# Kernel tuning notes

Measured on AMD Instinct MI355X. Metric: run time of the kernel, lower is better.

## Reference

```python
import jax, jax.numpy as jnp
import numpy as np


def setup_inputs() -> dict:
    key = jax.random.key(0)
    k1, k2, k3 = jax.random.split(key, 3)
    B, S, Q, K, D = 64, 512, 800, 4, 64
    q_data = jax.random.normal(k1, (B, S, Q), dtype=jnp.float32)
    r_data = jax.random.randint(k2, (B, S), 0, K)
    # learned params (xavier-ish scale)
    Wq = jax.random.normal(k3, (D, Q), dtype=jnp.float32) * (0.5 * (2.0 / (Q + D)) ** 0.5)
    bq = jnp.zeros((D,), dtype=jnp.float32)
    Wr = jax.random.normal(jax.random.fold_in(key, 7), (1, K), dtype=jnp.float32) * (0.5 * (2.0 / (K + 1)) ** 0.5)
    br = jnp.zeros((1,), dtype=jnp.float32)
    return {"q_data": q_data, "r_data": r_data, "Wq": Wq, "bq": bq,
            "Wr": Wr, "br": br, "n_questions": Q, "n_cats": K}


def reference(q_data, r_data, Wq, bq, Wr, br, n_questions, n_cats):
    # Vectorized over (batch, seq): original looped over t in python.
    K = n_cats
    k_idx = jnp.arange(K, dtype=q_data.dtype)                      # [K]
    dist = jnp.abs(k_idx[None, None, :] - r_data[..., None].astype(q_data.dtype)) / (K - 1)  # [B,S,K]
    weights = jnp.maximum(1.0 - dist, 0.0)                        # [B,S,K]
    # response_weights: Linear(K -> 1) then sigmoid -> scalar gate per (b,s)
    gate = jax.nn.sigmoid(jnp.einsum('bsk,ok->bso', weights, Wr) + br)  # [B,S,1]
    weighted_q = q_data * gate                                    # [B,S,Q]
    # question_embed: Linear(Q -> D)
    out = jnp.einsum('bsq,dq->bsd', weighted_q, Wq) + bq          # [B,S,D]
    return out
```

## Files before the change

### kernel.cpp

```cpp
#include <hip/hip_runtime.h>
#include <hip/hip_bf16.h>


#define QD 800
#define DD 64
#define M_TOTAL 32768
#define KT 25
#define DEPTH 5

typedef __attribute__((ext_vector_type(8))) short bf16x8;
typedef __attribute__((ext_vector_type(4))) float f32x4;

static __device__ __forceinline__ short f2bf(float f) {
  union { __hip_bfloat16 h; short s; } u;
  u.h = __float2bfloat16(f);
  return u.s;
}

static __device__ __forceinline__ bf16x8 pack8(f32x4 lo, f32x4 hi) {
  bf16x8 r;
  r[0] = f2bf(lo.x); r[1] = f2bf(lo.y); r[2] = f2bf(lo.z); r[3] = f2bf(lo.w);
  r[4] = f2bf(hi.x); r[5] = f2bf(hi.y); r[6] = f2bf(hi.z); r[7] = f2bf(hi.w);
  return r;
}

static __device__ __forceinline__ bf16x8 load_split8(const float* __restrict__ p) {
  return pack8(*reinterpret_cast<const f32x4*>(p),
               *reinterpret_cast<const f32x4*>(p + 16));
}

static __device__ __forceinline__ f32x4 ntload4(const float* __restrict__ p) {
  return __builtin_nontemporal_load(reinterpret_cast<const f32x4*>(p));
}

__global__ void convert_wq_kernel(const float* __restrict__ Wq, short* __restrict__ Bb) {
  int idx = blockIdx.x * 256 + threadIdx.x;
  int kt = idx >> 8;
  int acc = (idx >> 6) & 3;
  int lane = idx & 63;
  int l15 = lane & 15, lhi = lane >> 4;
  const float* p = Wq + (acc * 16 + l15) * QD + kt * 32 + lhi * 4;
  *reinterpret_cast<bf16x8*>(Bb + (size_t)idx * 8) = load_split8(p);
}

__global__ __launch_bounds__(256, 2) void sold_kernel(
    const float* __restrict__ q, const int* __restrict__ rdat,
    const short* __restrict__ Bb, const float* __restrict__ bq,
    const float* __restrict__ Wr, const float* __restrict__ br,
    float* __restrict__ out) {
  const int lane = threadIdx.x & 63;
  const int wave = threadIdx.x >> 6;
  const int l15 = lane & 15;
  const int lhi = lane >> 4;
  const int m0 = blockIdx.x * 64 + wave * 16;

  const float* ap = q + (size_t)(m0 + l15) * QD + lhi * 4;
  const short* bp = Bb + (size_t)lane * 8;

  f32x4 aLo[DEPTH], aHi[DEPTH];
  bf16x8 bfr[DEPTH][4];

#pragma unroll
  for (int s = 0; s < DEPTH; ++s) {
    const float* a = ap + s * 32;
    aLo[s] = ntload4(a);
    aHi[s] = ntload4(a + 16);
    const short* p = bp + s * 2048;
    bfr[s][0] = *reinterpret_cast<const bf16x8*>(p + 0 * 512);
    bfr[s][1] = *reinterpret_cast<const bf16x8*>(p + 1 * 512);
    bfr[s][2] = *reinterpret_cast<const bf16x8*>(p + 2 * 512);
    bfr[s][3] = *reinterpret_cast<const bf16x8*>(p + 3 * 512);
  }

  f32x4 acc0 = {0.f, 0.f, 0.f, 0.f};
  f32x4 acc1 = {0.f, 0.f, 0.f, 0.f};
  f32x4 acc2 = {0.f, 0.f, 0.f, 0.f};
  f32x4 acc3 = {0.f, 0.f, 0.f, 0.f};

#pragma unroll
  for (int kt = 0; kt < KT; ++kt) {
    const int s = kt % DEPTH;
    bf16x8 a = pack8(aLo[s], aHi[s]);
    acc0 = __builtin_amdgcn_mfma_f32_16x16x32_bf16(a, bfr[s][0], acc0, 0, 0, 0);
    acc1 = __builtin_amdgcn_mfma_f32_16x16x32_bf16(a, bfr[s][1], acc1, 0, 0, 0);
    acc2 = __builtin_amdgcn_mfma_f32_16x16x32_bf16(a, bfr[s][2], acc2, 0, 0, 0);
    acc3 = __builtin_amdgcn_mfma_f32_16x16x32_bf16(a, bfr[s][3], acc3, 0, 0, 0);
    const int nx = kt + DEPTH;
    if (nx < KT) {
      const float* a2 = ap + nx * 32;
      aLo[s] = ntload4(a2);
      aHi[s] = ntload4(a2 + 16);
      const short* p = bp + nx * 2048;
      bfr[s][0] = *reinterpret_cast<const bf16x8*>(p + 0 * 512);
      bfr[s][1] = *reinterpret_cast<const bf16x8*>(p + 1 * 512);
      bfr[s][2] = *reinterpret_cast<const bf16x8*>(p + 2 * 512);
      bfr[s][3] = *reinterpret_cast<const bf16x8*>(p + 3 * 512);
    }
    __builtin_amdgcn_sched_barrier(0);
  }

  float wr[4] = {Wr[0], Wr[1], Wr[2], Wr[3]};
  float brv = br[0];
  float lut[4];
  const float inv3 = 1.0f / 3.0f;
#pragma unroll
  for (int r = 0; r < 4; ++r) {
    float s = brv;
#pragma unroll
    for (int k = 0; k < 4; ++k) {
      float w = fmaxf(1.0f - fabsf((float)(k - r)) * inv3, 0.0f);
      s += w * wr[k];
    }
    lut[r] = 1.0f / (1.0f + __expf(-s));
  }

  float bqv0 = bq[0 * 16 + l15];
  float bqv1 = bq[1 * 16 + l15];
  float bqv2 = bq[2 * 16 + l15];
  float bqv3 = bq[3 * 16 + l15];

#pragma unroll
  for (int r = 0; r < 4; ++r) {
    int row = m0 + lhi * 4 + r;
    float g = lut[rdat[row]];
    float* orow = out + (size_t)row * DD + l15;
    __builtin_nontemporal_store(acc0[r] * g + bqv0, orow + 0);
    __builtin_nontemporal_store(acc1[r] * g + bqv1, orow + 16);
    __builtin_nontemporal_store(acc2[r] * g + bqv2, orow + 32);
    __builtin_nontemporal_store(acc3[r] * g + bqv3, orow + 48);
  }
}

__global__ __launch_bounds__(256, 2) void sold_direct(
    const float* __restrict__ q, const int* __restrict__ rdat,
    const float* __restrict__ Wq, const float* __restrict__ bq,
    const float* __restrict__ Wr, const float* __restrict__ br,
    float* __restrict__ out) {
  const int lane = threadIdx.x & 63;
  const int wave = threadIdx.x >> 6;
  const int l15 = lane & 15;
  const int lhi = lane >> 4;
  const int m0 = blockIdx.x * 64 + wave * 16;
  const float* aptr = q + (size_t)(m0 + l15) * QD + lhi * 4;
  const float* w0 = Wq + (0 * 16 + l15) * QD + lhi * 4;
  const float* w1 = Wq + (1 * 16 + l15) * QD + lhi * 4;
  const float* w2 = Wq + (2 * 16 + l15) * QD + lhi * 4;
  const float* w3 = Wq + (3 * 16 + l15) * QD + lhi * 4;
  f32x4 acc0 = {0.f,0.f,0.f,0.f}, acc1 = {0.f,0.f,0.f,0.f};
  f32x4 acc2 = {0.f,0.f,0.f,0.f}, acc3 = {0.f,0.f,0.f,0.f};
#pragma unroll 5
  for (int kt = 0; kt < KT; ++kt) {
    bf16x8 a  = load_split8(aptr + kt * 32);
    bf16x8 b0 = load_split8(w0 + kt * 32);
    bf16x8 b1 = load_split8(w1 + kt * 32);
    bf16x8 b2 = load_split8(w2 + kt * 32);
    bf16x8 b3 = load_split8(w3 + kt * 32);
    acc0 = __builtin_amdgcn_mfma_f32_16x16x32_bf16(a, b0, acc0, 0, 0, 0);
    acc1 = __builtin_amdgcn_mfma_f32_16x16x32_bf16(a, b1, acc1, 0, 0, 0);
    acc2 = __builtin_amdgcn_mfma_f32_16x16x32_bf16(a, b2, acc2, 0, 0, 0);
    acc3 = __builtin_amdgcn_mfma_f32_16x16x32_bf16(a, b3, acc3, 0, 0, 0);
  }
  float wr[4] = {Wr[0], Wr[1], Wr[2], Wr[3]};
  float brv = br[0], lut[4];
  const float inv3 = 1.0f / 3.0f;
#pragma unroll
  for (int r = 0; r < 4; ++r) {
    float s = brv;
#pragma unroll
    for (int k = 0; k < 4; ++k)
      s += fmaxf(1.0f - fabsf((float)(k - r)) * inv3, 0.0f) * wr[k];
    lut[r] = 1.0f / (1.0f + __expf(-s));
  }
  float bqv0 = bq[l15], bqv1 = bq[16 + l15], bqv2 = bq[32 + l15], bqv3 = bq[48 + l15];
#pragma unroll
  for (int r = 0; r < 4; ++r) {
    int row = m0 + lhi * 4 + r;
    float g = lut[rdat[row]];
    float* orow = out + (size_t)row * DD + l15;
    orow[0]  = acc0[r] * g + bqv0;
    orow[16] = acc1[r] * g + bqv1;
    orow[32] = acc2[r] * g + bqv2;
    orow[48] = acc3[r] * g + bqv3;
  }
}

extern "C" void kernel_launch(void* const* d_in, const int* in_sizes, int n_in,
                              void* d_out, int out_size, void* d_ws, size_t ws_size,
                              hipStream_t stream) {
  const float* q    = (const float*)d_in[0];
  const int*   rdat = (const int*)d_in[1];
  const float* Wq   = (const float*)d_in[2];
  const float* bq   = (const float*)d_in[3];
  const float* Wr   = (const float*)d_in[4];
  const float* br   = (const float*)d_in[5];
  float* out = (float*)d_out;

  const size_t need_ws = (size_t)KT * 2048 * sizeof(short);
  if (ws_size >= need_ws) {
    short* Bb = (short*)d_ws;
    convert_wq_kernel<<<KT, 256, 0, stream>>>(Wq, Bb);
    sold_kernel<<<M_TOTAL / 64, 256, 0, stream>>>(q, rdat, Bb, bq, Wr, br, out);
  } else {
    sold_direct<<<M_TOTAL / 64, 256, 0, stream>>>(q, rdat, Wq, bq, Wr, br, out);
  }
}
```

Measured before the change: 168.1 us.

## Stage bf16 Wq in LDS per block and drop the separate convert kernel

Removes the separate Wq-to-bf16 conversion kernel and its workspace buffer. Each 512-thread block now converts the whole Wq into LDS (100KB) itself, then streams B fragments from LDS with a 3-deep register prefetch while A keeps its 5-deep global prefetch. Block size and rows per block double to 128, which removes one launch and the global B reloads. The cost is that every block repeats the Wq conversion plus a sync before compute, and the large LDS footprint limits blocks per CU.

```diff
diff --git a/kernel.cpp b/kernel.cpp
--- a/kernel.cpp
+++ b/kernel.cpp
@@ -7,6 +7,7 @@
 #define M_TOTAL 32768
 #define KT 25
 #define DEPTH 5
+#define NCHUNK (KT * 4 * 64)
 
 typedef __attribute__((ext_vector_type(8))) short bf16x8;
 typedef __attribute__((ext_vector_type(4))) float f32x4;
@@ -33,44 +34,52 @@
   return __builtin_nontemporal_load(reinterpret_cast<const f32x4*>(p));
 }
 
-__global__ void convert_wq_kernel(const float* __restrict__ Wq, short* __restrict__ Bb) {
-  int idx = blockIdx.x * 256 + threadIdx.x;
-  int kt = idx >> 8;
-  int acc = (idx >> 6) & 3;
-  int lane = idx & 63;
-  int l15 = lane & 15, lhi = lane >> 4;
-  const float* p = Wq + (acc * 16 + l15) * QD + kt * 32 + lhi * 4;
-  *reinterpret_cast<bf16x8*>(Bb + (size_t)idx * 8) = load_split8(p);
-}
-
-__global__ __launch_bounds__(256, 2) void sold_kernel(
+__global__ __launch_bounds__(512, 2) void sold_lds(
     const float* __restrict__ q, const int* __restrict__ rdat,
-    const short* __restrict__ Bb, const float* __restrict__ bq,
+    const float* __restrict__ Wq, const float* __restrict__ bq,
     const float* __restrict__ Wr, const float* __restrict__ br,
     float* __restrict__ out) {
-  const int lane = threadIdx.x & 63;
-  const int wave = threadIdx.x >> 6;
+  __shared__ short Bs[NCHUNK * 8];
+
+  const int tid = threadIdx.x;
+
+#pragma unroll
+  for (int it = 0; it < 13; ++it) {
+    int idx = tid + it * 512;
+    if (idx < NCHUNK) {
+      int kt = idx >> 8;
+      int acc = (idx >> 6) & 3;
+      int cl = idx & 63;
+      int l15 = cl & 15, lhi = cl >> 4;
+      const float* p = Wq + (acc * 16 + l15) * QD + kt * 32 + lhi * 4;
+      *reinterpret_cast<bf16x8*>(&Bs[(size_t)idx * 8]) = load_split8(p);
+    }
+  }
+  __syncthreads();
+
+  const int lane = tid & 63;
+  const int wave = tid >> 6;
   const int l15 = lane & 15;
   const int lhi = lane >> 4;
-  const int m0 = blockIdx.x * 64 + wave * 16;
+  const int m0 = blockIdx.x * 128 + wave * 16;
 
   const float* ap = q + (size_t)(m0 + l15) * QD + lhi * 4;
-  const short* bp = Bb + (size_t)lane * 8;
+  const short* bp = Bs + lane * 8;
 
   f32x4 aLo[DEPTH], aHi[DEPTH];
-  bf16x8 bfr[DEPTH][4];
-
 #pragma unroll
   for (int s = 0; s < DEPTH; ++s) {
     const float* a = ap + s * 32;
     aLo[s] = ntload4(a);
     aHi[s] = ntload4(a + 16);
-    const short* p = bp + s * 2048;
-    bfr[s][0] = *reinterpret_cast<const bf16x8*>(p + 0 * 512);
-    bfr[s][1] = *reinterpret_cast<const bf16x8*>(p + 1 * 512);
-    bfr[s][2] = *reinterpret_cast<const bf16x8*>(p + 2 * 512);
-    bfr[s][3] = *reinterpret_cast<const bf16x8*>(p + 3 * 512);
   }
+
+  bf16x8 bb[3][4];
+#pragma unroll
+  for (int t = 0; t < 2; ++t)
+#pragma unroll
+    for (int j = 0; j < 4; ++j)
+      bb[t][j] = *reinterpret_cast<const bf16x8*>(bp + t * 2048 + j * 512);
 
   f32x4 acc0 = {0.f, 0.f, 0.f, 0.f};
   f32x4 acc1 = {0.f, 0.f, 0.f, 0.f};
@@ -79,22 +88,24 @@
 
 #pragma unroll
   for (int kt = 0; kt < KT; ++kt) {
-    const int s = kt % DEPTH;
-    bf16x8 a = pack8(aLo[s], aHi[s]);
-    acc0 = __builtin_amdgcn_mfma_f32_16x16x32_bf16(a, bfr[s][0], acc0, 0, 0, 0);
-    acc1 = __builtin_amdgcn_mfma_f32_16x16x32_bf16(a, bfr[s][1], acc1, 0, 0, 0);
-    acc2 = __builtin_amdgcn_mfma_f32_16x16x32_bf16(a, bfr[s][2], acc2, 0, 0, 0);
-    acc3 = __builtin_amdgcn_mfma_f32_16x16x32_bf16(a, bfr[s][3], acc3, 0, 0, 0);
+    const int cur = kt % 3;
+    const int pf = kt + 2;
+    if (pf < KT) {
+      const int dst = pf % 3;
+#pragma unroll
+      for (int j = 0; j < 4; ++j)
+        bb[dst][j] = *reinterpret_cast<const bf16x8*>(bp + pf * 2048 + j * 512);
+    }
+    bf16x8 a = pack8(aLo[kt % DEPTH], aHi[kt % DEPTH]);
+    acc0 = __builtin_amdgcn_mfma_f32_16x16x32_bf16(a, bb[cur][0], acc0, 0, 0, 0);
+    acc1 = __builtin_amdgcn_mfma_f32_16x16x32_bf16(a, bb[cur][1], acc1, 0, 0, 0);
+    acc2 = __builtin_amdgcn_mfma_f32_16x16x32_bf16(a, bb[cur][2], acc2, 0, 0, 0);
+    acc3 = __builtin_amdgcn_mfma_f32_16x16x32_bf16(a, bb[cur][3], acc3, 0, 0, 0);
     const int nx = kt + DEPTH;
     if (nx < KT) {
       const float* a2 = ap + nx * 32;
-      aLo[s] = ntload4(a2);
-      aHi[s] = ntload4(a2 + 16);
-      const short* p = bp + nx * 2048;
-      bfr[s][0] = *reinterpret_cast<const bf16x8*>(p + 0 * 512);
-      bfr[s][1] = *reinterpret_cast<const bf16x8*>(p + 1 * 512);
-      bfr[s][2] = *reinterpret_cast<const bf16x8*>(p + 2 * 512);
-      bfr[s][3] = *reinterpret_cast<const bf16x8*>(p + 3 * 512);
+      aLo[kt % DEPTH] = ntload4(a2);
+      aHi[kt % DEPTH] = ntload4(a2 + 16);
     }
     __builtin_amdgcn_sched_barrier(0);
   }
@@ -131,59 +142,6 @@
   }
 }
 
-__global__ __launch_bounds__(256, 2) void sold_direct(
-    const float* __restrict__ q, const int* __restrict__ rdat,
-    const float* __restrict__ Wq, const float* __restrict__ bq,
-    const float* __restrict__ Wr, const float* __restrict__ br,
-    float* __restrict__ out) {
-  const int lane = threadIdx.x & 63;
-  const int wave = threadIdx.x >> 6;
-  const int l15 = lane & 15;
-  const int lhi = lane >> 4;
-  const int m0 = blockIdx.x * 64 + wave * 16;
-  const float* aptr = q + (size_t)(m0 + l15) * QD + lhi * 4;
-  const float* w0 = Wq + (0 * 16 + l15) * QD + lhi * 4;
-  const float* w1 = Wq + (1 * 16 + l15) * QD + lhi * 4;
-  const float* w2 = Wq + (2 * 16 + l15) * QD + lhi * 4;
-  const float* w3 = Wq + (3 * 16 + l15) * QD + lhi * 4;
-  f32x4 acc0 = {0.f,0.f,0.f,0.f}, acc1 = {0.f,0.f,0.f,0.f};
-  f32x4 acc2 = {0.f,0.f,0.f,0.f}, acc3 = {0.f,0.f,0.f,0.f};
-#pragma unroll 5
-  for (int kt = 0; kt < KT; ++kt) {
-    bf16x8 a  = load_split8(aptr + kt * 32);
-    bf16x8 b0 = load_split8(w0 + kt * 32);
-    bf16x8 b1 = load_split8(w1 + kt * 32);
-    bf16x8 b2 = load_split8(w2 + kt * 32);
-    bf16x8 b3 = load_split8(w3 + kt * 32);
-    acc0 = __builtin_amdgcn_mfma_f32_16x16x32_bf16(a, b0, acc0, 0, 0, 0);
-    acc1 = __builtin_amdgcn_mfma_f32_16x16x32_bf16(a, b1, acc1, 0, 0, 0);
-    acc2 = __builtin_amdgcn_mfma_f32_16x16x32_bf16(a, b2, acc2, 0, 0, 0);
-    acc3 = __builtin_amdgcn_mfma_f32_16x16x32_bf16(a, b3, acc3, 0, 0, 0);
-  }
-  float wr[4] = {Wr[0], Wr[1], Wr[2], Wr[3]};
-  float brv = br[0], lut[4];
-  const float inv3 = 1.0f / 3.0f;
-#pragma unroll
-  for (int r = 0; r < 4; ++r) {
-    float s = brv;
-#pragma unroll
-    for (int k = 0; k < 4; ++k)
-      s += fmaxf(1.0f - fabsf((float)(k - r)) * inv3, 0.0f) * wr[k];
-    lut[r] = 1.0f / (1.0f + __expf(-s));
-  }
-  float bqv0 = bq[l15], bqv1 = bq[16 + l15], bqv2 = bq[32 + l15], bqv3 = bq[48 + l15];
-#pragma unroll
-  for (int r = 0; r < 4; ++r) {
-    int row = m0 + lhi * 4 + r;
-    float g = lut[rdat[row]];
-    float* orow = out + (size_t)row * DD + l15;
-    orow[0]  = acc0[r] * g + bqv0;
-    orow[16] = acc1[r] * g + bqv1;
-    orow[32] = acc2[r] * g + bqv2;
-    orow[48] = acc3[r] * g + bqv3;
-  }
-}
-
 extern "C" void kernel_launch(void* const* d_in, const int* in_sizes, int n_in,
                               void* d_out, int out_size, void* d_ws, size_t ws_size,
                               hipStream_t stream) {
@@ -195,12 +153,7 @@
   const float* br   = (const float*)d_in[5];
   float* out = (float*)d_out;
 
-  const size_t need_ws = (size_t)KT * 2048 * sizeof(short);
-  if (ws_size >= need_ws) {
-    short* Bb = (short*)d_ws;
-    convert_wq_kernel<<<KT, 256, 0, stream>>>(Wq, Bb);
-    sold_kernel<<<M_TOTAL / 64, 256, 0, stream>>>(q, rdat, Bb, bq, Wr, br, out);
-  } else {
-    sold_direct<<<M_TOTAL / 64, 256, 0, stream>>>(q, rdat, Wq, bq, Wr, br, out);
-  }
+  (void)d_ws; (void)ws_size;
+
+  sold_lds<<<M_TOTAL / 128, 512, 0, stream>>>(q, rdat, Wq, bq, Wr, br, out);
 }
```

After: 163.6 us. 2.7% less time.
